# Kernel optimization log

Measured on AMD Instinct MI355X. Metric: run time of the kernel, lower is better.

Reference implementation:

```python
import jax, jax.numpy as jnp
import numpy as np

B, S, D = 4, 2048, 1024


def setup_inputs() -> dict:
    key = jax.random.key(0)
    ks = jax.random.split(key, 7)
    s = 1.0 / np.sqrt(D)
    return {
        "x": jax.random.normal(ks[0], (B, S, D), dtype=jnp.float32),
        "Wq": jax.random.normal(ks[1], (D, D), dtype=jnp.float32) * s,
        "bq": jax.random.normal(ks[2], (D,), dtype=jnp.float32) * 0.01,
        "Wk": jax.random.normal(ks[3], (D, D), dtype=jnp.float32) * s,
        "bk": jax.random.normal(ks[4], (D,), dtype=jnp.float32) * 0.01,
        "Wv": jax.random.normal(ks[5], (D, D), dtype=jnp.float32) * s,
        "bv": jax.random.normal(ks[6], (D,), dtype=jnp.float32) * 0.01,
    }


def reference(x, Wq, bq, Wk, bk, Wv, bv):
    # x: [B, S, D]; Linear uses y = x @ W^T + b (torch convention)
    q = jnp.einsum("bsd,ed->bse", x, Wq) + bq
    k = jnp.einsum("bsd,ed->bse", x, Wk) + bk
    v = jnp.einsum("bsd,ed->bse", x, Wv) + bv
    # NOTE: original module applies softmax(q k^T) with NO 1/sqrt(d) scaling
    scores = jnp.einsum("bqd,bkd->bqk", q, k)  # [B, S, S]
    attn = jax.nn.softmax(scores, axis=-1)
    return jnp.einsum("bqk,bkd->bqd", attn, v)  # [B, S, D]
```

## Files before the change

kernel.cpp:

```cpp
#include <hip/hip_runtime.h>


#define Bb 4
#define Ss 2048
#define Dd 1024
#define Mtot 8192

typedef _Float16 f16x8 __attribute__((ext_vector_type(8)));
typedef float f32x4 __attribute__((ext_vector_type(4)));
typedef int i32x4 __attribute__((ext_vector_type(4)));
typedef signed char i8x16 __attribute__((ext_vector_type(16)));
typedef unsigned short u16;
typedef unsigned int u32;
typedef unsigned char u8;
typedef u16 u16x8 __attribute__((ext_vector_type(8)));
typedef u16 u16x4 __attribute__((ext_vector_type(4)));
typedef void __attribute__((address_space(1))) gvoid_t;
typedef void __attribute__((address_space(3))) svoid_t;

#define WC 1.953125e-3f
#define WCI 512.f
#define WFI 131072.f
#define W1S 7.62939453125e-6f
#define SG00 3.814697265625e-6f
#define SG01 1.4901161193847656e-8f
#define SG11 5.820766091346741e-11f

__device__ __forceinline__ void gl_lds16(const void* g, void* l) {
  __builtin_amdgcn_global_load_lds((gvoid_t*)g, (svoid_t*)l, 16, 0, 0);
}

__device__ __forceinline__ u16 f2h(float f) {
  return __builtin_bit_cast(u16, (_Float16)f);
}
__device__ __forceinline__ f16x8 frag_ld_h(const char* p) {
  u16x8 v = *(const u16x8*)p;
  return __builtin_bit_cast(f16x8, v);
}
__device__ __forceinline__ f32x4 mfma_f16(f16x8 a, f16x8 b, f32x4 c) {
  return __builtin_amdgcn_mfma_f32_16x16x32_f16(a, b, c, 0, 0, 0);
}
__device__ __forceinline__ i32x4 mfma_i8(i32x4 a, i32x4 b, i32x4 c) {
  return __builtin_amdgcn_mfma_i32_16x16x64_i8(a, b, c, 0, 0, 0);
}
__device__ __forceinline__ void dig2(float v, float cs, float ci, float fi,
                                     int& d0, int& d1) {
  float t = fminf(fmaxf(v * ci, -127.f), 127.f);
  d0 = __float2int_rn(t);
  float res = v - (float)d0 * cs;
  float u = fminf(fmaxf(res * fi, -127.f), 127.f);
  d1 = __float2int_rn(u);
}

template <int GX, int GY, int GZ>
__device__ __forceinline__ void xcd_swz(int& bx, int& by, int& bz) {
  constexpr int N = GX * GY * GZ;
  int flat = (int)blockIdx.x + GX * ((int)blockIdx.y + GY * (int)blockIdx.z);
  int s = (flat & 7) * (N >> 3) + (flat >> 3);
  bx = s & (GX - 1);
  by = (s / GX) & (GY - 1);
  bz = s / (GX * GY);
}

__device__ __forceinline__ void wait_bar_keep8() {
  asm volatile("s_waitcnt vmcnt(8)" ::: "memory");
  __builtin_amdgcn_s_barrier();
  __builtin_amdgcn_sched_barrier(0);
}
__device__ __forceinline__ void wait_bar_keep4() {
  asm volatile("s_waitcnt vmcnt(4)" ::: "memory");
  __builtin_amdgcn_s_barrier();
  __builtin_amdgcn_sched_barrier(0);
}
__device__ __forceinline__ void wait_bar_drain() {
  asm volatile("s_waitcnt vmcnt(0)" ::: "memory");
  __builtin_amdgcn_s_barrier();
  __builtin_amdgcn_sched_barrier(0);
}
__device__ __forceinline__ void end_bar() {
  __builtin_amdgcn_sched_barrier(0);
  __builtin_amdgcn_s_barrier();
}

template <int ROUNDS, int C>
__device__ __forceinline__ void stageF(const char* g, long row0, long ldb,
                                       long k0b, char* l, int tid) {
#pragma unroll
  for (int r = 0; r < ROUNDS; ++r) {
    int s = r * 256 + tid;
    int sub = s / (16 * C);
    int t = s % (16 * C);
    int h = t >> 6;
    int lk = (t >> 4) & 3;
    int lr = t & 15;
    gl_lds16(g + (row0 + sub * 16 + lr) * ldb + k0b + (h * 4 + lk) * 16,
             l + s * 16);
  }
}

__global__ void __launch_bounds__(256) convert_w(
    const float* __restrict__ Wq, const float* __restrict__ Wk,
    const float* __restrict__ Wv,
    u8* __restrict__ wq0, u8* __restrict__ wq1,
    u8* __restrict__ wk0, u8* __restrict__ wk1, u16* __restrict__ wvh) {
  long b = blockIdx.x;
  if (b < 2048) {
    int which = (int)(b >> 10);
    const float* src = which ? Wk : Wq;
    u8* o0 = which ? wk0 : wq0;
    u8* o1 = which ? wk1 : wq1;
    long i = (b & 1023) * 256 + threadIdx.x;
    f32x4 v = ((const f32x4*)src)[i];
    u32 p0 = 0, p1 = 0;
#pragma unroll
    for (int j = 0; j < 4; ++j) {
      int d0, d1;
      dig2(v[j], WC, WCI, WFI, d0, d1);
      p0 |= ((u32)(d0 & 255)) << (8 * j);
      p1 |= ((u32)(d1 & 255)) << (8 * j);
    }
    ((u32*)o0)[i] = p0;
    ((u32*)o1)[i] = p1;
  } else {
    long i = (b - 2048) * 256 + threadIdx.x;
    f32x4 v = ((const f32x4*)Wv)[i];
    u16x4 h;
#pragma unroll
    for (int j = 0; j < 4; ++j) h[j] = f2h(v[j]);
    ((u16x4*)wvh)[i] = h;
  }
}

__global__ void __launch_bounds__(256) transpose_w(
    const u8* __restrict__ wq0, const u8* __restrict__ wq1,
    const u8* __restrict__ wk0, const u8* __restrict__ wk1,
    u8* __restrict__ wqT0, u8* __restrict__ wqT1,
    u8* __restrict__ wkT0, u8* __restrict__ wkT1) {
  __shared__ u8 T[64][68];
  int a = blockIdx.z;
  const u8* src = a == 0 ? wq0 : a == 1 ? wq1 : a == 2 ? wk0 : wk1;
  u8* dst = a == 0 ? wqT0 : a == 1 ? wqT1 : a == 2 ? wkT0 : wkT1;
  int bi = blockIdx.y, bj = blockIdx.x;
  int t = threadIdx.x, r = t >> 2, c4 = t & 3;
  const u32* s = (const u32*)(src + (long)(bi * 64 + r) * 1024 + bj * 64 + c4 * 16);
  u32 v0 = s[0], v1 = s[1], v2 = s[2], v3 = s[3];
  u32* trow = (u32*)&T[r][c4 * 16];
  trow[0] = v0; trow[1] = v1; trow[2] = v2; trow[3] = v3;
  __syncthreads();
  u32 o[4] = {0, 0, 0, 0};
#pragma unroll
  for (int j = 0; j < 16; ++j)
    o[j >> 2] |= ((u32)T[c4 * 16 + j][r]) << (8 * (j & 3));
  u32* d = (u32*)(dst + (long)(bj * 64 + r) * 1024 + bi * 64 + c4 * 16);
  d[0] = o[0]; d[1] = o[1]; d[2] = o[2]; d[3] = o[3];
}

__global__ void __launch_bounds__(256) gvec_kernel(
    const u8* __restrict__ wqT0, const u8* __restrict__ wqT1,
    const u8* __restrict__ wkT0, const u8* __restrict__ wkT1,
    const float* __restrict__ bq, const float* __restrict__ bk,
    float* __restrict__ gq, float* __restrict__ gk, float* __restrict__ cbuf) {
  __shared__ float sbq[1024], sbk[1024];
  int tid = threadIdx.x;
  ((f32x4*)sbq)[tid] = ((const f32x4*)bq)[tid];
  ((f32x4*)sbk)[tid] = ((const f32x4*)bk)[tid];
  __syncthreads();
  int wave = tid >> 6, lane = tid & 63;
#pragma unroll
  for (int rr = 0; rr < 2; ++rr) {
    int d = blockIdx.x * 8 + wave * 2 + rr;
    i8x16 a0 = *(const i8x16*)(wqT0 + (long)d * 1024 + lane * 16);
    i8x16 a1 = *(const i8x16*)(wqT1 + (long)d * 1024 + lane * 16);
    i8x16 c0 = *(const i8x16*)(wkT0 + (long)d * 1024 + lane * 16);
    i8x16 c1 = *(const i8x16*)(wkT1 + (long)d * 1024 + lane * 16);
    float sq = 0.f, sk = 0.f;
#pragma unroll
    for (int j = 0; j < 16; ++j) {
      sq += ((float)a0[j] * WC + (float)a1[j] * W1S) * sbk[lane * 16 + j];
      sk += ((float)c0[j] * WC + (float)c1[j] * W1S) * sbq[lane * 16 + j];
    }
#pragma unroll
    for (int off = 32; off >= 1; off >>= 1) {
      sq += __shfl_xor(sq, off);
      sk += __shfl_xor(sk, off);
    }
    if (!lane) { gq[d] = sq; gk[d] = sk; }
  }
  if (blockIdx.x == 0 && wave == 0) {
    float c = 0.f;
#pragma unroll
    for (int j = 0; j < 16; ++j) c += sbq[lane * 16 + j] * sbk[lane * 16 + j];
#pragma unroll
    for (int off = 32; off >= 1; off >>= 1) c += __shfl_xor(c, off);
    if (!lane) cbuf[0] = c;
  }
}

__global__ void __launch_bounds__(256) convert_x(
    const float* __restrict__ x, const float* __restrict__ gq,
    const float* __restrict__ gk, const float* __restrict__ cbuf,
    u16* __restrict__ xh, float* __restrict__ ubuf, float* __restrict__ wbuf) {
  long b = blockIdx.x;
  int tid = threadIdx.x;
  long i = b * 256 + tid;
  f32x4 v = ((const f32x4*)x)[i];
  u16x4 h;
#pragma unroll
  for (int j = 0; j < 4; ++j) h[j] = f2h(v[j]);
  ((u16x4*)xh)[i] = h;

  f32x4 g4 = ((const f32x4*)gq)[tid];
  f32x4 k4 = ((const f32x4*)gk)[tid];
  float pu = v[0] * g4[0] + v[1] * g4[1] + v[2] * g4[2] + v[3] * g4[3];
  float pw = v[0] * k4[0] + v[1] * k4[1] + v[2] * k4[2] + v[3] * k4[3];
#pragma unroll
  for (int off = 32; off >= 1; off >>= 1) {
    pu += __shfl_xor(pu, off);
    pw += __shfl_xor(pw, off);
  }
  __shared__ float ru[4], rw[4];
  int wave = tid >> 6, lane = tid & 63;
  if (!lane) { ru[wave] = pu; rw[wave] = pw; }
  __syncthreads();
  if (!tid) {
    ubuf[b] = ru[0] + ru[1] + ru[2] + ru[3] + cbuf[0];
    wbuf[b] = rw[0] + rw[1] + rw[2] + rw[3];
  }
}

__global__ void __launch_bounds__(256, 2) g_part(
    const u8* __restrict__ wqT0, const u8* __restrict__ wqT1,
    const u8* __restrict__ wkT0, const u8* __restrict__ wkT1,
    float* __restrict__ Gpart) {
  __shared__ char lds[65536];
  const int tid = threadIdx.x;
  const int bx = blockIdx.x, by = blockIdx.y, bz = blockIdx.z;
  const long m0 = (long)by * 128;
  const int n0 = bx * 128;
  const int k00 = bz * 256;
  const int wave = tid >> 6, lane = tid & 63;
  const int wm = wave >> 1, wn = wave & 1;
  const int lr = lane & 15, lk = lane >> 4;

  i32x4 accM[4][4] = {};
  i32x4 accX[4][4] = {};
  i32x4 accY[4][4] = {};

  auto stage = [&](char* L, int kk) {
    stageF<2, 4>((const char*)wqT0, m0, 1024, kk, L + 0, tid);
    stageF<2, 4>((const char*)wqT1, m0, 1024, kk, L + 8192, tid);
    stageF<2, 4>((const char*)wkT0, n0, 1024, kk, L + 16384, tid);
    stageF<2, 4>((const char*)wkT1, n0, 1024, kk, L + 24576, tid);
  };
  auto compute = [&](const char* L) {
    i32x4 b0[4], b1[4];
#pragma unroll
    for (int nt = 0; nt < 4; ++nt) {
      int rb = (wn * 4 + nt) * 1024 + lane * 16;
      b0[nt] = *(const i32x4*)(L + 16384 + rb);
      b1[nt] = *(const i32x4*)(L + 24576 + rb);
    }
    __builtin_amdgcn_s_setprio(1);
#pragma unroll
    for (int mt = 0; mt < 4; ++mt) {
      int ra = (wm * 4 + mt) * 1024 + lane * 16;
      i32x4 a0 = *(const i32x4*)(L + ra);
      i32x4 a1 = *(const i32x4*)(L + 8192 + ra);
#pragma unroll
      for (int nt = 0; nt < 4; ++nt) {
        accM[mt][nt] = mfma_i8(a0, b0[nt], accM[mt][nt]);
        accX[mt][nt] = mfma_i8(a0, b1[nt], accX[mt][nt]);
        accX[mt][nt] = mfma_i8(a1, b0[nt], accX[mt][nt]);
        accY[mt][nt] = mfma_i8(a1, b1[nt], accY[mt][nt]);
      }
    }
    __builtin_amdgcn_s_setprio(0);
  };

  stage(lds, k00);
  for (int t = 0; t < 3; ++t) {
    char* L = lds + (t & 1) * 32768;
    stage(lds + ((t + 1) & 1) * 32768, k00 + (t + 1) * 64);
    wait_bar_keep8();
    compute(L);
    end_bar();
  }
  {
    char* L = lds + 32768;
    wait_bar_drain();
    compute(L);
  }

#pragma unroll
  for (int mt = 0; mt < 4; ++mt)
#pragma unroll
    for (int nt = 0; nt < 4; ++nt) {
      int e = n0 + wn * 64 + nt * 16 + lr;
      int gmb = (int)m0 + wm * 64 + mt * 16 + lk * 4;
      f32x4 o;
#pragma unroll
      for (int r = 0; r < 4; ++r)
        o[r] = (float)accM[mt][nt][r] * SG00 + (float)accX[mt][nt][r] * SG01 +
               (float)accY[mt][nt][r] * SG11;
      *(f32x4*)(Gpart + ((long)bz << 20) + (long)e * 1024 + gmb) = o;
    }
}

__global__ void __launch_bounds__(256) g_reduce(const float* __restrict__ Gpart,
                                                u16* __restrict__ Gh) {
  int n = blockIdx.x, tid = threadIdx.x;
  long o = (long)n * 1024 + tid * 4;
  f32x4 v = *(const f32x4*)(Gpart + o);
  f32x4 v1 = *(const f32x4*)(Gpart + (1L << 20) + o);
  f32x4 v2 = *(const f32x4*)(Gpart + (2L << 20) + o);
  f32x4 v3 = *(const f32x4*)(Gpart + (3L << 20) + o);
  u16x4 h;
#pragma unroll
  for (int j = 0; j < 4; ++j) h[j] = f2h(v[j] + v1[j] + v2[j] + v3[j]);
  ((u16x4*)Gh)[n * 256 + tid] = h;
}

__global__ void __launch_bounds__(256) t_gemm(
    const u16* __restrict__ xh, const u16* __restrict__ Gh,
    u16* __restrict__ th) {
  __shared__ char lds[65536];
  const int tid = threadIdx.x;
  int bx, by, bz;
  xcd_swz<8, 64, 1>(bx, by, bz);
  const long m0 = (long)by * 128;
  const int n0 = bx * 128;
  const int wave = tid >> 6, lane = tid & 63;
  const int wm = wave >> 1, wn = wave & 1;
  const int lr = lane & 15, lk = lane >> 4;

  f32x4 acc[4][4] = {};

  auto stage = [&](char* L, int k0) {
    stageF<4, 8>((const char*)xh, m0, (long)Dd * 2, (long)k0 * 2, L + 0, tid);
    stageF<4, 8>((const char*)Gh, n0, (long)Dd * 2, (long)k0 * 2, L + 16384, tid);
  };
  auto compute = [&](const char* L) {
    f16x8 af[2][4], bfr[2][4];
#pragma unroll
    for (int ks = 0; ks < 2; ++ks)
#pragma unroll
      for (int i = 0; i < 4; ++i) {
        af[ks][i] = frag_ld_h(L + (wm * 4 + i) * 2048 + ks * 1024 + lane * 16);
        bfr[ks][i] = frag_ld_h(L + 16384 + (wn * 4 + i) * 2048 + ks * 1024 + lane * 16);
      }
    __builtin_amdgcn_s_setprio(1);
#pragma unroll
    for (int ks = 0; ks < 2; ++ks)
#pragma unroll
      for (int mt = 0; mt < 4; ++mt)
#pragma unroll
        for (int nt = 0; nt < 4; ++nt)
          acc[mt][nt] = mfma_f16(af[ks][mt], bfr[ks][nt], acc[mt][nt]);
    __builtin_amdgcn_s_setprio(0);
  };

  stage(lds, 0);
  for (int t = 0; t < Dd / 64 - 1; ++t) {
    char* L = lds + (t & 1) * 32768;
    stage(lds + ((t + 1) & 1) * 32768, (t + 1) * 64);
    wait_bar_keep8();
    compute(L);
    end_bar();
  }
  {
    char* L = lds + ((Dd / 64 - 1) & 1) * 32768;
    wait_bar_drain();
    compute(L);
  }

#pragma unroll
  for (int mt = 0; mt < 4; ++mt)
#pragma unroll
    for (int nt = 0; nt < 4; ++nt)
#pragma unroll
      for (int r = 0; r < 4; ++r) {
        long gm = m0 + wm * 64 + mt * 16 + lk * 4 + r;
        int e = n0 + wn * 64 + nt * 16 + lr;
        th[gm * Dd + e] = f2h(acc[mt][nt][r]);
      }
}

__global__ void __launch_bounds__(256) v_gemm(
    const u16* __restrict__ xh, const u16* __restrict__ wvh,
    const float* __restrict__ bv, u16* __restrict__ vt) {
  __shared__ char lds[65536];
  const int tid = threadIdx.x;
  int bx, by, bz;
  xcd_swz<8, 64, 1>(bx, by, bz);
  const long m0 = (long)by * 128;
  const int n0 = bx * 128;
  const int wave = tid >> 6, lane = tid & 63;
  const int wm = wave >> 1, wn = wave & 1;
  const int lr = lane & 15, lk = lane >> 4;

  f32x4 acc[4][4] = {};

  auto stage = [&](char* L, int k0) {
    stageF<4, 8>((const char*)xh, m0, (long)Dd * 2, (long)k0 * 2, L + 0, tid);
    stageF<4, 8>((const char*)wvh, n0, (long)Dd * 2, (long)k0 * 2, L + 16384, tid);
  };
  auto compute = [&](const char* L) {
    f16x8 af[2][4], bfr[2][4];
#pragma unroll
    for (int ks = 0; ks < 2; ++ks)
#pragma unroll
      for (int i = 0; i < 4; ++i) {
        af[ks][i] = frag_ld_h(L + (wm * 4 + i) * 2048 + ks * 1024 + lane * 16);
        bfr[ks][i] = frag_ld_h(L + 16384 + (wn * 4 + i) * 2048 + ks * 1024 + lane * 16);
      }
    __builtin_amdgcn_s_setprio(1);
#pragma unroll
    for (int ks = 0; ks < 2; ++ks)
#pragma unroll
      for (int mt = 0; mt < 4; ++mt)
#pragma unroll
        for (int nt = 0; nt < 4; ++nt)
          acc[mt][nt] = mfma_f16(af[ks][mt], bfr[ks][nt], acc[mt][nt]);
    __builtin_amdgcn_s_setprio(0);
  };

  stage(lds, 0);
  for (int t = 0; t < Dd / 64 - 1; ++t) {
    char* L = lds + (t & 1) * 32768;
    stage(lds + ((t + 1) & 1) * 32768, (t + 1) * 64);
    wait_bar_keep8();
    compute(L);
    end_bar();
  }
  {
    char* L = lds + ((Dd / 64 - 1) & 1) * 32768;
    wait_bar_drain();
    compute(L);
  }

#pragma unroll
  for (int mt = 0; mt < 4; ++mt)
#pragma unroll
    for (int nt = 0; nt < 4; ++nt)
#pragma unroll
      for (int r = 0; r < 4; ++r) {
        long gm = m0 + wm * 64 + mt * 16 + lk * 4 + r;
        int e = n0 + wn * 64 + nt * 16 + lr;
        float v = acc[mt][nt][r] + bv[e];
        long b = gm >> 11, s = gm & 2047;
        vt[(b * Dd + e) * (long)Ss + s] = f2h(v);
      }
}

__global__ void __launch_bounds__(256, 4) score_gemm(
    const u16* __restrict__ th, const u16* __restrict__ xh,
    const float* __restrict__ ubuf, const float* __restrict__ wbuf,
    float* __restrict__ scores) {
  __shared__ char lds[32768];
  const int tid = threadIdx.x;
  int bx, by, bz;
  xcd_swz<16, 16, 4>(bx, by, bz);
  const int z = bz;
  const long base = (long)z * Ss * Dd * 2;
  const long m0 = (long)by * 128;
  const int n0 = bx * 128;
  const int wave = tid >> 6, lane = tid & 63;
  const int wm = wave >> 1, wn = wave & 1;
  const int lr = lane & 15, lk = lane >> 4;

  f32x4 acc[4][4] = {};

  auto stage = [&](char* L, int k0) {
    stageF<2, 4>((const char*)th + base, m0, (long)Dd * 2, (long)k0 * 2, L + 0, tid);
    stageF<2, 4>((const char*)xh + base, n0, (long)Dd * 2, (long)k0 * 2, L + 8192, tid);
  };
  auto compute = [&](const char* L) {
    f16x8 af[4], bfr[4];
#pragma unroll
    for (int i = 0; i < 4; ++i) {
      af[i] = frag_ld_h(L + (wm * 4 + i) * 1024 + lane * 16);
      bfr[i] = frag_ld_h(L + 8192 + (wn * 4 + i) * 1024 + lane * 16);
    }
    __builtin_amdgcn_s_setprio(1);
#pragma unroll
    for (int mt = 0; mt < 4; ++mt)
#pragma unroll
      for (int nt = 0; nt < 4; ++nt)
        acc[mt][nt] = mfma_f16(af[mt], bfr[nt], acc[mt][nt]);
    __builtin_amdgcn_s_setprio(0);
  };

  stage(lds, 0);
  for (int t = 0; t < Dd / 32 - 1; ++t) {
    char* L = lds + (t & 1) * 16384;
    stage(lds + ((t + 1) & 1) * 16384, (t + 1) * 32);
    wait_bar_keep4();
    compute(L);
    end_bar();
  }
  {
    char* L = lds + ((Dd / 32 - 1) & 1) * 16384;
    wait_bar_drain();
    compute(L);
  }

  float* srow = scores + (long)z * Ss * Ss;
#pragma unroll
  for (int mt = 0; mt < 4; ++mt)
#pragma unroll
    for (int nt = 0; nt < 4; ++nt)
#pragma unroll
      for (int r = 0; r < 4; ++r) {
        long i = m0 + wm * 64 + mt * 16 + lk * 4 + r;
        int j = n0 + wn * 64 + nt * 16 + lr;
        srow[i * Ss + j] = acc[mt][nt][r] +
                           ubuf[(z << 11) + i] + wbuf[(z << 11) + j];
      }
}

__global__ void __launch_bounds__(256) softmax_rows(const float* __restrict__ scores,
                                                    u16* __restrict__ P) {
  const long r = blockIdx.x;
  const float* row = scores + r * Ss;
  u16* prow = P + r * Ss;
  const int t = threadIdx.x;
  const int wave = t >> 6, lane = t & 63;
  f32x4 v0 = ((const f32x4*)row)[t * 2];
  f32x4 v1 = ((const f32x4*)row)[t * 2 + 1];
  float a[8];
#pragma unroll
  for (int j = 0; j < 4; ++j) { a[j] = v0[j]; a[4 + j] = v1[j]; }

  float m = a[0];
#pragma unroll
  for (int j = 1; j < 8; ++j) m = fmaxf(m, a[j]);
#pragma unroll
  for (int off = 32; off >= 1; off >>= 1) m = fmaxf(m, __shfl_xor(m, off));
  __shared__ float red[4];
  if (lane == 0) red[wave] = m;
  __syncthreads();
  m = fmaxf(fmaxf(red[0], red[1]), fmaxf(red[2], red[3]));

  float e[8];
  float s = 0.f;
#pragma unroll
  for (int j = 0; j < 8; ++j) { e[j] = __expf(a[j] - m); s += e[j]; }
#pragma unroll
  for (int off = 32; off >= 1; off >>= 1) s += __shfl_xor(s, off);
  __syncthreads();
  if (lane == 0) red[wave] = s;
  __syncthreads();
  s = red[0] + red[1] + red[2] + red[3];
  float inv = 1.0f / s;

  u16x8 pk;
#pragma unroll
  for (int j = 0; j < 8; ++j) pk[j] = f2h(e[j] * inv);
  ((u16x8*)prow)[t] = pk;
}

__global__ void __launch_bounds__(256) pv_gemm(const u16* __restrict__ P,
                                               const u16* __restrict__ vt,
                                               float* __restrict__ out) {
  __shared__ char lds[65536];
  const int tid = threadIdx.x;
  int bx, by, bz;
  xcd_swz<8, 16, 4>(bx, by, bz);
  const int z = bz;
  const u16* A = P + (long)z * Ss * Ss;
  const u16* Bp = vt + (long)z * Dd * Ss;
  const long m0 = (long)by * 128;
  const int n0 = bx * 128;

  const int wave = tid >> 6, lane = tid & 63;
  const int wm = wave >> 1, wn = wave & 1;
  const int lr = lane & 15, lk = lane >> 4;

  f32x4 acc[4][4] = {};

  auto stage = [&](char* L, int k0) {
    stageF<4, 8>((const char*)A, m0, (long)Ss * 2, (long)k0 * 2, L + 0, tid);
    stageF<4, 8>((const char*)Bp, n0, (long)Ss * 2, (long)k0 * 2, L + 16384, tid);
  };
  auto compute = [&](const char* L) {
    f16x8 af[2][4], bfr[2][4];
#pragma unroll
    for (int ks = 0; ks < 2; ++ks)
#pragma unroll
      for (int i = 0; i < 4; ++i) {
        af[ks][i] = frag_ld_h(L + (wm * 4 + i) * 2048 + ks * 1024 + lane * 16);
        bfr[ks][i] = frag_ld_h(L + 16384 + (wn * 4 + i) * 2048 + ks * 1024 + lane * 16);
      }
    __builtin_amdgcn_s_setprio(1);
#pragma unroll
    for (int ks = 0; ks < 2; ++ks)
#pragma unroll
      for (int mt = 0; mt < 4; ++mt)
#pragma unroll
        for (int nt = 0; nt < 4; ++nt)
          acc[mt][nt] = mfma_f16(af[ks][mt], bfr[ks][nt], acc[mt][nt]);
    __builtin_amdgcn_s_setprio(0);
  };

  stage(lds, 0);
  for (int t = 0; t < Ss / 64 - 1; ++t) {
    char* L = lds + (t & 1) * 32768;
    stage(lds + ((t + 1) & 1) * 32768, (t + 1) * 64);
    wait_bar_keep8();
    compute(L);
    end_bar();
  }
  {
    char* L = lds + ((Ss / 64 - 1) & 1) * 32768;
    wait_bar_drain();
    compute(L);
  }

  float* orow = out + (long)z * Ss * Dd;
#pragma unroll
  for (int mt = 0; mt < 4; ++mt)
#pragma unroll
    for (int nt = 0; nt < 4; ++nt)
#pragma unroll
      for (int r = 0; r < 4; ++r) {
        long i = m0 + wm * 64 + mt * 16 + lk * 4 + r;
        int e = n0 + wn * 64 + nt * 16 + lr;
        orow[i * Dd + e] = acc[mt][nt][r];
      }
}

extern "C" void kernel_launch(void* const* d_in, const int* in_sizes, int n_in,
                              void* d_out, int out_size, void* d_ws, size_t ws_size,
                              hipStream_t stream) {
  const float* x = (const float*)d_in[0];
  const float* Wq = (const float*)d_in[1];
  const float* bq = (const float*)d_in[2];
  const float* Wk = (const float*)d_in[3];
  const float* bk = (const float*)d_in[4];
  const float* Wv = (const float*)d_in[5];
  const float* bv = (const float*)d_in[6];
  float* out = (float*)d_out;

  char* p = (char*)d_ws;
  float* scores = (float*)p;
  u16* Gh = (u16*)p;
  u16* wvh = (u16*)(p + (16L << 20));
  u16* th = (u16*)(p + (80L << 20));
  u8* wq0 = (u8*)(p + (80L << 20));
  u8* wq1 = wq0 + (1L << 20);
  u8* wk0 = wq0 + (2L << 20);
  u8* wk1 = wq0 + (3L << 20);
  float* Gpart = (float*)(p + (80L << 20));
  u16* Pbuf = (u16*)(p + (96L << 20));
  u16* xh = (u16*)(p + (96L << 20));
  u16* vt = (u16*)(p + (128L << 20));
  u8* wqT0 = (u8*)(p + (144L << 20));
  u8* wqT1 = wqT0 + (1L << 20);
  u8* wkT0 = wqT0 + (2L << 20);
  u8* wkT1 = wqT0 + (3L << 20);
  float* gq = (float*)(p + (148L << 20));
  float* gk = gq + 1024;
  float* ubuf = gq + 2048;
  float* wbuf = ubuf + 8192;
  float* cbuf = wbuf + 8192;

  convert_w<<<dim3(3072), dim3(256), 0, stream>>>(Wq, Wk, Wv, wq0, wq1, wk0, wk1, wvh);
  transpose_w<<<dim3(16, 16, 4), dim3(256), 0, stream>>>(
      wq0, wq1, wk0, wk1, wqT0, wqT1, wkT0, wkT1);
  gvec_kernel<<<dim3(128), dim3(256), 0, stream>>>(
      wqT0, wqT1, wkT0, wkT1, bq, bk, gq, gk, cbuf);
  convert_x<<<dim3(8192), dim3(256), 0, stream>>>(
      x, gq, gk, cbuf, xh, ubuf, wbuf);
  v_gemm<<<dim3(Dd / 128, Mtot / 128), dim3(256), 0, stream>>>(xh, wvh, bv, vt);
  g_part<<<dim3(8, 8, 4), dim3(256), 0, stream>>>(wqT0, wqT1, wkT0, wkT1, Gpart);
  g_reduce<<<dim3(1024), dim3(256), 0, stream>>>(Gpart, Gh);
  t_gemm<<<dim3(Dd / 128, Mtot / 128), dim3(256), 0, stream>>>(xh, Gh, th);
  score_gemm<<<dim3(Ss / 128, Ss / 128, Bb), dim3(256), 0, stream>>>(
      th, xh, ubuf, wbuf, scores);
  softmax_rows<<<dim3(Bb * Ss), dim3(256), 0, stream>>>(scores, Pbuf);
  pv_gemm<<<dim3(Dd / 128, Ss / 128, Bb), dim3(256), 0, stream>>>(Pbuf, vt, out);
}
```

Before: 348.4 us.

## Unify f16 GEMMs into a triple-buffered K=32 pipeline core with higher occupancy

Replaces the per-kernel double-buffered GEMM loops with a shared core that stages K=32 tiles into three LDS buffers, keeping two loads in flight while computing. The 64-wide-K kernels (t, v, pv) drop from 64KB to 48KB LDS and gain launch bounds allowing two blocks per CU. The score GEMM moves from a double-buffered 32KB setup at 4 blocks per CU to the 48KB triple buffer at 3 blocks per CU. The intent is to hide global-load latency better. The cost is more barriers per unit of K work and reduced occupancy for the score kernel.

```diff
diff --git a/kernel.cpp b/kernel.cpp
--- a/kernel.cpp
+++ b/kernel.cpp
@@ -96,6 +96,49 @@
     gl_lds16(g + (row0 + sub * 16 + lr) * ldb + k0b + (h * 4 + lk) * 16,
              l + s * 16);
   }
+}
+
+template <int NT>
+__device__ __forceinline__ void gemm_f16_core(
+    const char* A, const char* B, long m0, long n0, long lda, long ldb,
+    char* lds, int tid, int wm, int wn, int lane, f32x4 (&acc)[4][4]) {
+  auto stage = [&](char* L, int t) {
+    stageF<2, 4>(A, m0, lda, (long)t * 64, L, tid);
+    stageF<2, 4>(B, n0, ldb, (long)t * 64, L + 8192, tid);
+  };
+  auto compute = [&](const char* L) {
+    f16x8 af[4], bfr[4];
+#pragma unroll
+    for (int i = 0; i < 4; ++i) {
+      af[i] = frag_ld_h(L + (wm * 4 + i) * 1024 + lane * 16);
+      bfr[i] = frag_ld_h(L + 8192 + (wn * 4 + i) * 1024 + lane * 16);
+    }
+    __builtin_amdgcn_s_setprio(1);
+#pragma unroll
+    for (int mt = 0; mt < 4; ++mt)
+#pragma unroll
+      for (int nt = 0; nt < 4; ++nt)
+        acc[mt][nt] = mfma_f16(af[mt], bfr[nt], acc[mt][nt]);
+    __builtin_amdgcn_s_setprio(0);
+  };
+
+  char* L0 = lds;
+  char* L1 = lds + 16384;
+  char* L2 = lds + 32768;
+  stage(L0, 0);
+  stage(L1, 1);
+  for (int t = 0; t < NT - 2; ++t) {
+    stage(L2, t + 2);
+    wait_bar_keep8();
+    compute(L0);
+    end_bar();
+    char* tmp = L0; L0 = L1; L1 = L2; L2 = tmp;
+  }
+  wait_bar_keep4();
+  compute(L0);
+  end_bar();
+  wait_bar_drain();
+  compute(L1);
 }
 
 __global__ void __launch_bounds__(256) convert_w(
@@ -320,10 +363,10 @@
   ((u16x4*)Gh)[n * 256 + tid] = h;
 }
 
-__global__ void __launch_bounds__(256) t_gemm(
+__global__ void __launch_bounds__(256, 2) t_gemm(
     const u16* __restrict__ xh, const u16* __restrict__ Gh,
     u16* __restrict__ th) {
-  __shared__ char lds[65536];
+  __shared__ char lds[49152];
   const int tid = threadIdx.x;
   int bx, by, bz;
   xcd_swz<8, 64, 1>(bx, by, bz);
@@ -334,44 +377,8 @@
   const int lr = lane & 15, lk = lane >> 4;
 
   f32x4 acc[4][4] = {};
-
-  auto stage = [&](char* L, int k0) {
-    stageF<4, 8>((const char*)xh, m0, (long)Dd * 2, (long)k0 * 2, L + 0, tid);
-    stageF<4, 8>((const char*)Gh, n0, (long)Dd * 2, (long)k0 * 2, L + 16384, tid);
-  };
-  auto compute = [&](const char* L) {
-    f16x8 af[2][4], bfr[2][4];
-#pragma unroll
-    for (int ks = 0; ks < 2; ++ks)
-#pragma unroll
-      for (int i = 0; i < 4; ++i) {
-        af[ks][i] = frag_ld_h(L + (wm * 4 + i) * 2048 + ks * 1024 + lane * 16);
-        bfr[ks][i] = frag_ld_h(L + 16384 + (wn * 4 + i) * 2048 + ks * 1024 + lane * 16);
-      }
-    __builtin_amdgcn_s_setprio(1);
-#pragma unroll
-    for (int ks = 0; ks < 2; ++ks)
-#pragma unroll
-      for (int mt = 0; mt < 4; ++mt)
-#pragma unroll
-        for (int nt = 0; nt < 4; ++nt)
-          acc[mt][nt] = mfma_f16(af[ks][mt], bfr[ks][nt], acc[mt][nt]);
-    __builtin_amdgcn_s_setprio(0);
-  };
-
-  stage(lds, 0);
-  for (int t = 0; t < Dd / 64 - 1; ++t) {
-    char* L = lds + (t & 1) * 32768;
-    stage(lds + ((t + 1) & 1) * 32768, (t + 1) * 64);
-    wait_bar_keep8();
-    compute(L);
-    end_bar();
-  }
-  {
-    char* L = lds + ((Dd / 64 - 1) & 1) * 32768;
-    wait_bar_drain();
-    compute(L);
-  }
+  gemm_f16_core<32>((const char*)xh, (const char*)Gh, m0, n0,
+                    (long)Dd * 2, (long)Dd * 2, lds, tid, wm, wn, lane, acc);
 
 #pragma unroll
   for (int mt = 0; mt < 4; ++mt)
@@ -385,10 +392,10 @@
       }
 }
 
-__global__ void __launch_bounds__(256) v_gemm(
+__global__ void __launch_bounds__(256, 2) v_gemm(
     const u16* __restrict__ xh, const u16* __restrict__ wvh,
     const float* __restrict__ bv, u16* __restrict__ vt) {
-  __shared__ char lds[65536];
+  __shared__ char lds[49152];
   const int tid = threadIdx.x;
   int bx, by, bz;
   xcd_swz<8, 64, 1>(bx, by, bz);
@@ -399,44 +406,8 @@
   const int lr = lane & 15, lk = lane >> 4;
 
   f32x4 acc[4][4] = {};
-
-  auto stage = [&](char* L, int k0) {
-    stageF<4, 8>((const char*)xh, m0, (long)Dd * 2, (long)k0 * 2, L + 0, tid);
-    stageF<4, 8>((const char*)wvh, n0, (long)Dd * 2, (long)k0 * 2, L + 16384, tid);
-  };
-  auto compute = [&](const char* L) {
-    f16x8 af[2][4], bfr[2][4];
-#pragma unroll
-    for (int ks = 0; ks < 2; ++ks)
-#pragma unroll
-      for (int i = 0; i < 4; ++i) {
-        af[ks][i] = frag_ld_h(L + (wm * 4 + i) * 2048 + ks * 1024 + lane * 16);
-        bfr[ks][i] = frag_ld_h(L + 16384 + (wn * 4 + i) * 2048 + ks * 1024 + lane * 16);
-      }
-    __builtin_amdgcn_s_setprio(1);
-#pragma unroll
-    for (int ks = 0; ks < 2; ++ks)
-#pragma unroll
-      for (int mt = 0; mt < 4; ++mt)
-#pragma unroll
-        for (int nt = 0; nt < 4; ++nt)
-          acc[mt][nt] = mfma_f16(af[ks][mt], bfr[ks][nt], acc[mt][nt]);
-    __builtin_amdgcn_s_setprio(0);
-  };
-
-  stage(lds, 0);
-  for (int t = 0; t < Dd / 64 - 1; ++t) {
-    char* L = lds + (t & 1) * 32768;
-    stage(lds + ((t + 1) & 1) * 32768, (t + 1) * 64);
-    wait_bar_keep8();
-    compute(L);
-    end_bar();
-  }
-  {
-    char* L = lds + ((Dd / 64 - 1) & 1) * 32768;
-    wait_bar_drain();
-    compute(L);
-  }
+  gemm_f16_core<32>((const char*)xh, (const char*)wvh, m0, n0,
+                    (long)Dd * 2, (long)Dd * 2, lds, tid, wm, wn, lane, acc);
 
 #pragma unroll
   for (int mt = 0; mt < 4; ++mt)
@@ -452,11 +423,11 @@
       }
 }
 
-__global__ void __launch_bounds__(256, 4) score_gemm(
+__global__ void __launch_bounds__(256, 3) score_gemm(
     const u16* __restrict__ th, const u16* __restrict__ xh,
     const float* __restrict__ ubuf, const float* __restrict__ wbuf,
     float* __restrict__ scores) {
-  __shared__ char lds[32768];
+  __shared__ char lds[49152];
   const int tid = threadIdx.x;
   int bx, by, bz;
   xcd_swz<16, 16, 4>(bx, by, bz);
@@ -469,40 +440,8 @@
   const int lr = lane & 15, lk = lane >> 4;
 
   f32x4 acc[4][4] = {};
-
-  auto stage = [&](char* L, int k0) {
-    stageF<2, 4>((const char*)th + base, m0, (long)Dd * 2, (long)k0 * 2, L + 0, tid);
-    stageF<2, 4>((const char*)xh + base, n0, (long)Dd * 2, (long)k0 * 2, L + 8192, tid);
-  };
-  auto compute = [&](const char* L) {
-    f16x8 af[4], bfr[4];
-#pragma unroll
-    for (int i = 0; i < 4; ++i) {
-      af[i] = frag_ld_h(L + (wm * 4 + i) * 1024 + lane * 16);
-      bfr[i] = frag_ld_h(L + 8192 + (wn * 4 + i) * 1024 + lane * 16);
-    }
-    __builtin_amdgcn_s_setprio(1);
-#pragma unroll
-    for (int mt = 0; mt < 4; ++mt)
-#pragma unroll
-      for (int nt = 0; nt < 4; ++nt)
-        acc[mt][nt] = mfma_f16(af[mt], bfr[nt], acc[mt][nt]);
-    __builtin_amdgcn_s_setprio(0);
-  };
-
-  stage(lds, 0);
-  for (int t = 0; t < Dd / 32 - 1; ++t) {
-    char* L = lds + (t & 1) * 16384;
-    stage(lds + ((t + 1) & 1) * 16384, (t + 1) * 32);
-    wait_bar_keep4();
-    compute(L);
-    end_bar();
-  }
-  {
-    char* L = lds + ((Dd / 32 - 1) & 1) * 16384;
-    wait_bar_drain();
-    compute(L);
-  }
+  gemm_f16_core<32>((const char*)th + base, (const char*)xh + base, m0, n0,
+                    (long)Dd * 2, (long)Dd * 2, lds, tid, wm, wn, lane, acc);
 
   float* srow = scores + (long)z * Ss * Ss;
 #pragma unroll
@@ -559,16 +498,16 @@
   ((u16x8*)prow)[t] = pk;
 }
 
-__global__ void __launch_bounds__(256) pv_gemm(const u16* __restrict__ P,
-                                               const u16* __restrict__ vt,
-                                               float* __restrict__ out) {
-  __shared__ char lds[65536];
+__global__ void __launch_bounds__(256, 2) pv_gemm(const u16* __restrict__ P,
+                                                  const u16* __restrict__ vt,
+                                                  float* __restrict__ out) {
+  __shared__ char lds[49152];
   const int tid = threadIdx.x;
   int bx, by, bz;
   xcd_swz<8, 16, 4>(bx, by, bz);
   const int z = bz;
-  const u16* A = P + (long)z * Ss * Ss;
-  const u16* Bp = vt + (long)z * Dd * Ss;
+  const char* A = (const char*)(P + (long)z * Ss * Ss);
+  const char* Bp = (const char*)(vt + (long)z * Dd * Ss);
   const long m0 = (long)by * 128;
   const int n0 = bx * 128;
 
@@ -577,44 +516,8 @@
   const int lr = lane & 15, lk = lane >> 4;
 
   f32x4 acc[4][4] = {};
-
-  auto stage = [&](char* L, int k0) {
-    stageF<4, 8>((const char*)A, m0, (long)Ss * 2, (long)k0 * 2, L + 0, tid);
-    stageF<4, 8>((const char*)Bp, n0, (long)Ss * 2, (long)k0 * 2, L + 16384, tid);
-  };
-  auto compute = [&](const char* L) {
-    f16x8 af[2][4], bfr[2][4];
-#pragma unroll
-    for (int ks = 0; ks < 2; ++ks)
-#pragma unroll
-      for (int i = 0; i < 4; ++i) {
-        af[ks][i] = frag_ld_h(L + (wm * 4 + i) * 2048 + ks * 1024 + lane * 16);
-        bfr[ks][i] = frag_ld_h(L + 16384 + (wn * 4 + i) * 2048 + ks * 1024 + lane * 16);
-      }
-    __builtin_amdgcn_s_setprio(1);
-#pragma unroll
-    for (int ks = 0; ks < 2; ++ks)
-#pragma unroll
-      for (int mt = 0; mt < 4; ++mt)
-#pragma unroll
-        for (int nt = 0; nt < 4; ++nt)
-          acc[mt][nt] = mfma_f16(af[ks][mt], bfr[ks][nt], acc[mt][nt]);
-    __builtin_amdgcn_s_setprio(0);
-  };
-
-  stage(lds, 0);
-  for (int t = 0; t < Ss / 64 - 1; ++t) {
-    char* L = lds + (t & 1) * 32768;
-    stage(lds + ((t + 1) & 1) * 32768, (t + 1) * 64);
-    wait_bar_keep8();
-    compute(L);
-    end_bar();
-  }
-  {
-    char* L = lds + ((Ss / 64 - 1) & 1) * 32768;
-    wait_bar_drain();
-    compute(L);
-  }
+  gemm_f16_core<64>(A, Bp, m0, n0, (long)Ss * 2, (long)Ss * 2,
+                    lds, tid, wm, wn, lane, acc);
 
   float* orow = out + (long)z * Ss * Dd;
 #pragma unroll
```

Result: faster. 337.5 us (-3.1%).
